# Kernel optimization log

Measured on AMD Instinct MI355X. Metric: run time of the kernel, lower is better.

Reference implementation:

```python
import jax, jax.numpy as jnp
from jax import lax
import numpy as np

GROUPS = 4


def _grid_sample_border(img, gx, gy):
    # img: [Bg, Cg, H, W]; gx, gy: [Bg, H, W] normalized grid in [-1, 1]
    # Replicates F.grid_sample(mode='bilinear', align_corners=False, padding_mode='border')
    Bg, Cg, H, W = img.shape
    ix = jnp.clip(((gx + 1.0) * W - 1.0) * 0.5, 0.0, W - 1.0)
    iy = jnp.clip(((gy + 1.0) * H - 1.0) * 0.5, 0.0, H - 1.0)
    x0 = jnp.floor(ix)
    y0 = jnp.floor(iy)
    wx = ix - x0
    wy = iy - y0
    x0i = x0.astype(jnp.int32)
    y0i = y0.astype(jnp.int32)
    x1i = jnp.minimum(x0i + 1, W - 1)
    y1i = jnp.minimum(y0i + 1, H - 1)

    def one(im, x0i, x1i, y0i, y1i, wx, wy):
        v00 = im[:, y0i, x0i]
        v01 = im[:, y0i, x1i]
        v10 = im[:, y1i, x0i]
        v11 = im[:, y1i, x1i]
        return (v00 * (1 - wx) * (1 - wy) + v01 * wx * (1 - wy)
                + v10 * (1 - wx) * wy + v11 * wx * wy)

    return jax.vmap(one)(img, x0i, x1i, y0i, y1i, wx, wy)


def setup_inputs() -> dict:
    key = jax.random.key(0)
    ks = jax.random.split(key, 8)
    B, N, C = 8, 4096, 768
    x = jax.random.normal(ks[0], (B, N, C), dtype=jnp.float32)
    dw_w = jax.random.normal(ks[1], (C, 1, 3, 3), dtype=jnp.float32) * 0.1  # depthwise kernel
    dw_b = jax.random.normal(ks[2], (C,), dtype=jnp.float32) * 0.1
    off_w = jax.random.normal(ks[3], (2 * GROUPS, C), dtype=jnp.float32) * 0.001  # std=0.001 init
    off_b = jnp.zeros((2 * GROUPS,), dtype=jnp.float32)
    wt_w = jax.random.normal(ks[4], (2 * GROUPS, C), dtype=jnp.float32) * 0.02
    wt_b = jnp.zeros((2 * GROUPS,), dtype=jnp.float32)
    offset_list = jnp.zeros((1,), dtype=jnp.int32)
    return {"x": x, "dw_w": dw_w, "dw_b": dw_b, "off_w": off_w, "off_b": off_b,
            "wt_w": wt_w, "wt_b": wt_b, "offset_list": offset_list,
            "patch_h": 64, "patch_w": 64}


def reference(x, dw_w, dw_b, off_w, off_b, wt_w, wt_b, offset_list, patch_h, patch_w):
    B, N, C = x.shape
    H, W = int(patch_h), int(patch_w)
    xi = jnp.transpose(x, (0, 2, 1)).reshape(B, C, H, W)

    # offset head: depthwise 3x3 conv -> GELU -> 1x1 conv to 2*groups channels
    dw = lax.conv_general_dilated(xi, dw_w, (1, 1), ((1, 1), (1, 1)),
                                  dimension_numbers=("NCHW", "OIHW", "NCHW"),
                                  feature_group_count=C)
    dw = jax.nn.gelu(dw + dw_b[None, :, None, None], approximate=False)
    off = jnp.einsum("bchw,oc->bohw", dw, off_w) + off_b[None, :, None, None]

    # weight head: 1x1 conv -> sigmoid
    wt = jax.nn.sigmoid(jnp.einsum("bchw,oc->bohw", xi, wt_w) + wt_b[None, :, None, None])

    off = (off * wt).reshape(B, 2, GROUPS, H, W)
    # fixed cross-shaped shifts: x-comp [0,0,-1,+1], y-comp [-1,+1,0,0]
    shifts = jnp.array([[0.0, 0.0, -1.0, 1.0], [-1.0, 1.0, 0.0, 0.0]],
                       dtype=x.dtype).reshape(1, 2, GROUPS, 1, 1)
    off = off + shifts

    cx = (jnp.arange(W, dtype=x.dtype) + 0.5)[None, None, None, :]  # pixel-center x coords
    cy = (jnp.arange(H, dtype=x.dtype) + 0.5)[None, None, :, None]  # pixel-center y coords
    gx = 2.0 * (cx + off[:, 0]) / W - 1.0  # [B, GROUPS, H, W]
    gy = 2.0 * (cy + off[:, 1]) / H - 1.0

    img = xi.reshape(B * GROUPS, C // GROUPS, H, W)
    samp = _grid_sample_border(img, gx.reshape(B * GROUPS, H, W),
                               gy.reshape(B * GROUPS, H, W))
    out = samp.reshape(B, C, N)
    return jnp.transpose(out, (0, 2, 1))  # [B, N, C]
```

## Files before the change

kernel.cpp:

```cpp
#include <hip/hip_runtime.h>
#include <math.h>

#define BB 8
#define CC 768
#define HH 64
#define WW 64
#define NN 4096
#define GG 4
#define NCHUNK 6
#define CHUNK 128

typedef __attribute__((ext_vector_type(8))) _Float16 half8;
typedef __attribute__((ext_vector_type(4))) float f32x4;

__device__ __forceinline__ float gelu_fast(float v) {
    const float z = 1.5957691216f * v * fmaf(0.044715f, v * v, 1.0f);
    return __fdividef(v, 1.0f + __expf(-z));
}

__global__ __launch_bounds__(128, 4) void dq_conv_mfma(
    const float* __restrict__ x,
    const float* __restrict__ dw_w,
    const float* __restrict__ dw_b,
    const float* __restrict__ off_w,
    const float* __restrict__ wt_w,
    float* __restrict__ offpart)
{
    __shared__ __attribute__((aligned(16))) _Float16 gl[16][144];
    __shared__ __attribute__((aligned(16))) _Float16 xh[16][144];
    const int t = threadIdx.x;
    const int lane = t & 63, wv = t >> 6;
    const int xcd = blockIdx.x & 7;
    const int local = blockIdx.x >> 3;
    const int chunk = local % NCHUNK;
    const int r = xcd * (BB * HH / 8) + local / NCHUNK;
    const int h = r & (HH - 1);
    const int b = r >> 6;
    const int c = chunk * CHUNK + t;

    const int n = lane & 15, kg = lane >> 4;
    const float* wsrc = (wv == 0) ? off_w : wt_w;
    half8 bfrag[4];
#pragma unroll
    for (int kt = 0; kt < 4; ++kt) {
        const bool valid = (n < 8);
        const float* src = wsrc + (valid ? n : 0) * CC + chunk * CHUNK + kt * 32 + kg * 8;
        half8 bf;
#pragma unroll
        for (int j = 0; j < 8; ++j) {
            bf[j] = (_Float16)(valid ? src[j] : 0.f);
        }
        bfrag[kt] = bf;
    }

    float w9[9];
#pragma unroll
    for (int j = 0; j < 9; ++j) w9[j] = dw_w[c * 9 + j];
    const float bias = dw_b[c];
    const bool tv = (h > 0), bv = (h < HH - 1);
    const float wt0 = tv ? w9[0] : 0.f, wt1 = tv ? w9[1] : 0.f, wt2 = tv ? w9[2] : 0.f;
    const float wb0 = bv ? w9[6] : 0.f, wb1 = bv ? w9[7] : 0.f, wb2 = bv ? w9[8] : 0.f;

    const float* base = x + (size_t)b * NN * CC + c;
    const float* rT = base + (size_t)((tv ? h - 1 : 0) * WW) * CC;
    const float* rM = base + (size_t)(h * WW) * CC;
    const float* rB = base + (size_t)((bv ? h + 1 : h) * WW) * CC;

    float cT[8], cM[8], cB[8], nT[8], nM[8], nB[8];
    float pT = 0.f, pM = 0.f, pB = 0.f;

#pragma unroll
    for (int j = 0; j < 8; ++j) {
        const size_t o = (size_t)j * CC;
        cT[j] = rT[o]; cM[j] = rM[o]; cB[j] = rB[o];
    }

#pragma unroll 1
    for (int wb = 0; wb < 8; ++wb) {
        if (wb < 7) {
#pragma unroll
            for (int j = 0; j < 8; ++j) {
                const size_t o = (size_t)(8 + j) * CC;
                nT[j] = rT[o]; nM[j] = rM[o]; nB[j] = rB[o];
            }
        } else {
#pragma unroll
            for (int j = 0; j < 8; ++j) { nT[j] = 0.f; nM[j] = 0.f; nB[j] = 0.f; }
        }
#pragma unroll
        for (int j = 0; j < 8; ++j) {
            const float lT = j ? cT[j - 1] : pT;
            const float lM = j ? cM[j - 1] : pM;
            const float lB = j ? cB[j - 1] : pB;
            const float rTv = (j == 7) ? nT[0] : cT[j + 1];
            const float rMv = (j == 7) ? nM[0] : cM[j + 1];
            const float rBv = (j == 7) ? nB[0] : cB[j + 1];
            const float conv = lT * wt0 + cT[j] * wt1 + rTv * wt2
                             + lM * w9[3] + cM[j] * w9[4] + rMv * w9[5]
                             + lB * wb0 + cB[j] * wb1 + rBv * wb2;
            const int colq = ((wb & 1) << 3) + j;
            gl[colq][t] = (_Float16)gelu_fast(conv + bias);
            xh[colq][t] = (_Float16)cM[j];
        }
        pT = cT[7]; pM = cM[7]; pB = cB[7];
#pragma unroll
        for (int j = 0; j < 8; ++j) { cT[j] = nT[j]; cM[j] = nM[j]; cB[j] = nB[j]; }
        rT += 8 * CC; rM += 8 * CC; rB += 8 * CC;

        if (wb & 1) {
            const int q = wb >> 1;
            __syncthreads();
            f32x4 acc = {0.f, 0.f, 0.f, 0.f};
            if (wv == 0) {
#pragma unroll
                for (int kt = 0; kt < 4; ++kt) {
                    const half8 a = *(const half8*)&gl[n][kt * 32 + kg * 8];
                    acc = __builtin_amdgcn_mfma_f32_16x16x32_f16(a, bfrag[kt], acc, 0, 0, 0);
                }
            } else {
#pragma unroll
                for (int kt = 0; kt < 4; ++kt) {
                    const half8 a = *(const half8*)&xh[n][kt * 32 + kg * 8];
                    acc = __builtin_amdgcn_mfma_f32_16x16x32_f16(a, bfrag[kt], acc, 0, 0, 0);
                }
            }
            if (n < 8) {
                const int plane = chunk * 16 + (wv ? 8 + n : n);
                const size_t gpos = (size_t)(b * NN) + h * WW + q * 16 + kg * 4;
                float4 st; st.x = acc[0]; st.y = acc[1]; st.z = acc[2]; st.w = acc[3];
                *(float4*)&offpart[(size_t)plane * (BB * NN) + gpos] = st;
            }
            if (wb < 7) __syncthreads();
        }
    }
}

__global__ __launch_bounds__(256) void dq_combine(
    const float* __restrict__ offpart,
    const float* __restrict__ off_b,
    const float* __restrict__ wt_b,
    float* __restrict__ ixiy)
{
    const int t = threadIdx.x;
    const int o = t >> 5;
    const int gpos = blockIdx.x * 32 + (t & 31);
    const int b = gpos >> 12;
    const int hw = gpos & 4095;
    const int h = hw >> 6, w = hw & 63;

    float so = 0.f, sw = 0.f;
#pragma unroll
    for (int ch = 0; ch < NCHUNK; ++ch) {
        so += offpart[((size_t)(ch * 16 + o)) * (BB * NN) + gpos];
        sw += offpart[((size_t)(ch * 16 + 8 + o)) * (BB * NN) + gpos];
    }
    const float sig = 1.f / (1.f + __expf(-(sw + wt_b[o])));
    const float val = (so + off_b[o]) * sig;

    if (o < 4) {
        const float shx = (o == 2) ? -1.f : ((o == 3) ? 1.f : 0.f);
        const float ix = fminf(fmaxf((float)w + val + shx, 0.f), (float)(WW - 1));
        ixiy[(b * GG + o) * NN + hw] = ix;
    } else {
        const int g = o - 4;
        const float shy = (g == 0) ? -1.f : ((g == 1) ? 1.f : 0.f);
        const float iy = fminf(fmaxf((float)h + val + shy, 0.f), (float)(HH - 1));
        ixiy[BB * GG * NN + (b * GG + g) * NN + hw] = iy;
    }
}

__global__ __launch_bounds__(192) void dq_sample_vec(
    const float* __restrict__ x,
    const float* __restrict__ ixiy,
    float* __restrict__ out)
{
    __shared__ float ixy[8];
    const int t = threadIdx.x;
    const int p = (blockIdx.x & 7) * (BB * NN / 8) + (blockIdx.x >> 3);
    const int b = p >> 12;
    const int hw = p & 4095;

    if (t < 8) {
        const int g = t & 3;
        const int plane = (t >> 2) * (BB * GG * NN);
        ixy[t] = ixiy[plane + (b * GG + g) * NN + hw];
    }
    __syncthreads();

    const int g = t / 48;
    const float ix = ixy[g], iy = ixy[4 + g];
    const float x0f = floorf(ix), y0f = floorf(iy);
    const float wx = ix - x0f, wy = iy - y0f;
    const int x0 = (int)x0f, y0 = (int)y0f;
    const int x1 = min(x0 + 1, WW - 1), y1 = min(y0 + 1, HH - 1);
    const int c4 = t * 4;
    const float* xb = x + (size_t)b * NN * CC;
    const float4 v00 = *(const float4*)(xb + (size_t)(y0 * WW + x0) * CC + c4);
    const float4 v01 = *(const float4*)(xb + (size_t)(y0 * WW + x1) * CC + c4);
    const float4 v10 = *(const float4*)(xb + (size_t)(y1 * WW + x0) * CC + c4);
    const float4 v11 = *(const float4*)(xb + (size_t)(y1 * WW + x1) * CC + c4);
    const float w00 = (1.f - wx) * (1.f - wy), w01 = wx * (1.f - wy);
    const float w10 = (1.f - wx) * wy,         w11 = wx * wy;
    float4 r;
    r.x = v00.x * w00 + v01.x * w01 + v10.x * w10 + v11.x * w11;
    r.y = v00.y * w00 + v01.y * w01 + v10.y * w10 + v11.y * w11;
    r.z = v00.z * w00 + v01.z * w01 + v10.z * w10 + v11.z * w11;
    r.w = v00.w * w00 + v01.w * w01 + v10.w * w10 + v11.w * w11;
    *(float4*)(out + (size_t)p * CC + c4) = r;
}

__global__ __launch_bounds__(256) void dqshift_offsets_kernel(
    const float* __restrict__ x, const float* __restrict__ dw_w,
    const float* __restrict__ dw_b, const float* __restrict__ off_w,
    const float* __restrict__ off_b, const float* __restrict__ wt_w,
    const float* __restrict__ wt_b, float* __restrict__ ixiy)
{
    const int wave = threadIdx.x >> 6;
    const int lane = threadIdx.x & 63;
    const int p = blockIdx.x * 4 + wave;
    const int b = p >> 12;
    const int hw = p & 4095;
    const int h = hw >> 6;
    const int w = hw & 63;
    const float* xb = x + (size_t)b * NN * CC;
    float accO[8], accW[8];
#pragma unroll
    for (int o = 0; o < 8; ++o) { accO[o] = 0.f; accW[o] = 0.f; }
    for (int k = 0; k < CC / 64; ++k) {
        const int c = lane + (k << 6);
        float conv = 0.f, xc = 0.f;
#pragma unroll
        for (int dy = -1; dy <= 1; ++dy) {
            const int hh = h + dy;
            const bool vy = (hh >= 0) && (hh < HH);
#pragma unroll
            for (int dx = -1; dx <= 1; ++dx) {
                const int ww = w + dx;
                const bool vv = vy && (ww >= 0) && (ww < WW);
                const float tt = vv ? xb[(size_t)(hh * WW + ww) * CC + c] : 0.f;
                if (dy == 0 && dx == 0) xc = tt;
                conv = fmaf(tt, dw_w[c * 9 + (dy + 1) * 3 + (dx + 1)], conv);
            }
        }
        const float gv = conv + dw_b[c];
        const float gle = 0.5f * gv * (1.0f + erff(gv * 0.70710678118654752f));
#pragma unroll
        for (int o = 0; o < 8; ++o) {
            accO[o] = fmaf(gle, off_w[o * CC + c], accO[o]);
            accW[o] = fmaf(xc, wt_w[o * CC + c], accW[o]);
        }
    }
#pragma unroll
    for (int o = 0; o < 8; ++o) {
#pragma unroll
        for (int s = 32; s > 0; s >>= 1) {
            accO[o] += __shfl_xor(accO[o], s, 64);
            accW[o] += __shfl_xor(accW[o], s, 64);
        }
    }
    if (lane == 0) {
        const float shx[4] = {0.f, 0.f, -1.f, 1.f};
        const float shy[4] = {-1.f, 1.f, 0.f, 0.f};
#pragma unroll
        for (int g = 0; g < 4; ++g) {
            const float sx = 1.f / (1.f + expf(-(accW[g] + wt_b[g])));
            const float sy = 1.f / (1.f + expf(-(accW[4 + g] + wt_b[4 + g])));
            const float ox = (accO[g] + off_b[g]) * sx + shx[g];
            const float oy = (accO[4 + g] + off_b[4 + g]) * sy + shy[g];
            const float ix = fminf(fmaxf((float)w + ox, 0.f), (float)(WW - 1));
            const float iy = fminf(fmaxf((float)h + oy, 0.f), (float)(HH - 1));
            const int idx = (b * GG + g) * NN + hw;
            ixiy[idx] = ix;
            ixiy[BB * GG * NN + idx] = iy;
        }
    }
}

__global__ __launch_bounds__(256) void dqshift_sample_kernel(
    const float* __restrict__ x,
    const float* __restrict__ ixiy,
    float* __restrict__ out)
{
    const int p = blockIdx.x;
    const int b = p >> 12;
    const int hw = p & 4095;
    const float* xb = x + (size_t)b * NN * CC;
    float* ob = out + (size_t)p * CC;

#pragma unroll
    for (int k = 0; k < 3; ++k) {
        const int c = threadIdx.x + (k << 8);
        const int g = c / (CC / GG);
        const int idx = (b * GG + g) * NN + hw;
        const float ix = ixiy[idx];
        const float iy = ixiy[BB * GG * NN + idx];
        const float x0f = floorf(ix);
        const float y0f = floorf(iy);
        const float wx = ix - x0f;
        const float wy = iy - y0f;
        const int x0 = (int)x0f;
        const int y0 = (int)y0f;
        const int x1 = min(x0 + 1, WW - 1);
        const int y1 = min(y0 + 1, HH - 1);
        const float* r0 = xb + (size_t)(y0 * WW) * CC + c;
        const float* r1 = xb + (size_t)(y1 * WW) * CC + c;
        const float v00 = r0[(size_t)x0 * CC];
        const float v01 = r0[(size_t)x1 * CC];
        const float v10 = r1[(size_t)x0 * CC];
        const float v11 = r1[(size_t)x1 * CC];
        ob[c] = v00 * (1.f - wx) * (1.f - wy) + v01 * wx * (1.f - wy)
              + v10 * (1.f - wx) * wy + v11 * wx * wy;
    }
}

extern "C" void kernel_launch(void* const* d_in, const int* in_sizes, int n_in,
                              void* d_out, int out_size, void* d_ws, size_t ws_size,
                              hipStream_t stream) {
    const float* x     = (const float*)d_in[0];
    const float* dw_w  = (const float*)d_in[1];
    const float* dw_b  = (const float*)d_in[2];
    const float* off_w = (const float*)d_in[3];
    const float* off_b = (const float*)d_in[4];
    const float* wt_w  = (const float*)d_in[5];
    const float* wt_b  = (const float*)d_in[6];

    float* ixiy = (float*)d_ws;
    float* offpart = (float*)d_ws + 2 * BB * GG * NN;
    const size_t need = (size_t)(2 * BB * GG * NN + NCHUNK * 16 * BB * NN) * 4;

    if (ws_size >= need) {
        dq_conv_mfma<<<BB * HH * NCHUNK, 128, 0, stream>>>(
            x, dw_w, dw_b, off_w, wt_w, offpart);
        dq_combine<<<BB * NN / 32, 256, 0, stream>>>(
            offpart, off_b, wt_b, ixiy);
        dq_sample_vec<<<BB * NN, 192, 0, stream>>>(
            x, ixiy, (float*)d_out);
    } else {
        dqshift_offsets_kernel<<<BB * NN / 4, 256, 0, stream>>>(
            x, dw_w, dw_b, off_w, off_b, wt_w, wt_b, ixiy);
        dqshift_sample_kernel<<<BB * NN, 256, 0, stream>>>(x, ixiy, (float*)d_out);
    }
}
```

Measured before the change: 82.40 us.

## Process two channels per thread and split conv rows into half-width blocks

The depthwise-conv/MFMA kernel now handles 256 channels per block with each thread loading float2 pairs, and splits each image row into two 32-column halves, which need halo loads at the split edge. The grid grows from 3072 to 3072 blocks (3 chunks × 2 halves), the MFMA K loop doubles to 8 tiles, and the combine kernel reads 3 partial chunks instead of 6. GELU now uses exp2 directly. The intent is to widen global loads, halve the partial-sum traffic, and shorten each block's serial column loop, at the cost of more registers per thread and lower launch-bound occupancy.

```diff
diff --git a/kernel.cpp b/kernel.cpp
--- a/kernel.cpp
+++ b/kernel.cpp
@@ -7,18 +7,20 @@
 #define WW 64
 #define NN 4096
 #define GG 4
-#define NCHUNK 6
-#define CHUNK 128
+#define NCHUNK 3
+#define CHUNK 256
 
 typedef __attribute__((ext_vector_type(8))) _Float16 half8;
+typedef __attribute__((ext_vector_type(2))) _Float16 half2f;
 typedef __attribute__((ext_vector_type(4))) float f32x4;
 
 __device__ __forceinline__ float gelu_fast(float v) {
-    const float z = 1.5957691216f * v * fmaf(0.044715f, v * v, 1.0f);
-    return __fdividef(v, 1.0f + __expf(-z));
-}
-
-__global__ __launch_bounds__(128, 4) void dq_conv_mfma(
+    const float z2 = 2.3022223f * v * fmaf(0.044715f, v * v, 1.0f);
+    const float e = __builtin_amdgcn_exp2f(-z2);
+    return __fdividef(v, 1.0f + e);
+}
+
+__global__ __launch_bounds__(128, 3) void dq_conv_mfma(
     const float* __restrict__ x,
     const float* __restrict__ dw_w,
     const float* __restrict__ dw_b,
@@ -26,107 +28,125 @@
     const float* __restrict__ wt_w,
     float* __restrict__ offpart)
 {
-    __shared__ __attribute__((aligned(16))) _Float16 gl[16][144];
-    __shared__ __attribute__((aligned(16))) _Float16 xh[16][144];
+    __shared__ __attribute__((aligned(16))) _Float16 gl[16][272];
+    __shared__ __attribute__((aligned(16))) _Float16 xh[16][272];
     const int t = threadIdx.x;
     const int lane = t & 63, wv = t >> 6;
     const int xcd = blockIdx.x & 7;
-    const int local = blockIdx.x >> 3;
-    const int chunk = local % NCHUNK;
-    const int r = xcd * (BB * HH / 8) + local / NCHUNK;
+    int local = blockIdx.x >> 3;
+    const int chunk = local % 3; local /= 3;
+    const int half = local & 1;  local >>= 1;
+    const int r = xcd * (BB * HH / 8) + local;
     const int h = r & (HH - 1);
     const int b = r >> 6;
-    const int c = chunk * CHUNK + t;
+    const int wstart = half * 32;
+    const int c0 = chunk * CHUNK + 2 * t;
 
     const int n = lane & 15, kg = lane >> 4;
     const float* wsrc = (wv == 0) ? off_w : wt_w;
-    half8 bfrag[4];
-#pragma unroll
-    for (int kt = 0; kt < 4; ++kt) {
+    half8 bfrag[8];
+#pragma unroll
+    for (int kt = 0; kt < 8; ++kt) {
         const bool valid = (n < 8);
         const float* src = wsrc + (valid ? n : 0) * CC + chunk * CHUNK + kt * 32 + kg * 8;
         half8 bf;
 #pragma unroll
-        for (int j = 0; j < 8; ++j) {
-            bf[j] = (_Float16)(valid ? src[j] : 0.f);
-        }
+        for (int j = 0; j < 8; ++j) bf[j] = (_Float16)(valid ? src[j] : 0.f);
         bfrag[kt] = bf;
     }
 
-    float w9[9];
-#pragma unroll
-    for (int j = 0; j < 9; ++j) w9[j] = dw_w[c * 9 + j];
-    const float bias = dw_b[c];
+    float wA[9], wB[9];
+#pragma unroll
+    for (int j = 0; j < 9; ++j) { wA[j] = dw_w[c0 * 9 + j]; wB[j] = dw_w[(c0 + 1) * 9 + j]; }
+    const float biasA = dw_b[c0], biasB = dw_b[c0 + 1];
     const bool tv = (h > 0), bv = (h < HH - 1);
-    const float wt0 = tv ? w9[0] : 0.f, wt1 = tv ? w9[1] : 0.f, wt2 = tv ? w9[2] : 0.f;
-    const float wb0 = bv ? w9[6] : 0.f, wb1 = bv ? w9[7] : 0.f, wb2 = bv ? w9[8] : 0.f;
-
-    const float* base = x + (size_t)b * NN * CC + c;
+    if (!tv) { wA[0] = wA[1] = wA[2] = 0.f; wB[0] = wB[1] = wB[2] = 0.f; }
+    if (!bv) { wA[6] = wA[7] = wA[8] = 0.f; wB[6] = wB[7] = wB[8] = 0.f; }
+
+    const float* base = x + (size_t)b * NN * CC + c0;
     const float* rT = base + (size_t)((tv ? h - 1 : 0) * WW) * CC;
     const float* rM = base + (size_t)(h * WW) * CC;
     const float* rB = base + (size_t)((bv ? h + 1 : h) * WW) * CC;
 
-    float cT[8], cM[8], cB[8], nT[8], nM[8], nB[8];
-    float pT = 0.f, pM = 0.f, pB = 0.f;
-
-#pragma unroll
-    for (int j = 0; j < 8; ++j) {
-        const size_t o = (size_t)j * CC;
-        cT[j] = rT[o]; cM[j] = rM[o]; cB[j] = rB[o];
-    }
-
-#pragma unroll 1
+    float2 cT[4], cM[4], cB[4], nT[4], nM[4], nB[4];
+    float2 pT, pM, pB;
+    const float2 zz = make_float2(0.f, 0.f);
+    if (half) {
+        const size_t o = (size_t)(wstart - 1) * CC;
+        pT = *(const float2*)&rT[o]; pM = *(const float2*)&rM[o]; pB = *(const float2*)&rB[o];
+    } else { pT = zz; pM = zz; pB = zz; }
+    float2 tT, tM, tB;
+    if (!half) {
+        const size_t o = (size_t)(wstart + 32) * CC;
+        tT = *(const float2*)&rT[o]; tM = *(const float2*)&rM[o]; tB = *(const float2*)&rB[o];
+    } else { tT = zz; tM = zz; tB = zz; }
+
+#pragma unroll
+    for (int j = 0; j < 4; ++j) {
+        const size_t o = (size_t)(wstart + j) * CC;
+        cT[j] = *(const float2*)&rT[o]; cM[j] = *(const float2*)&rM[o]; cB[j] = *(const float2*)&rB[o];
+    }
+
+#pragma unroll
     for (int wb = 0; wb < 8; ++wb) {
         if (wb < 7) {
 #pragma unroll
-            for (int j = 0; j < 8; ++j) {
-                const size_t o = (size_t)(8 + j) * CC;
-                nT[j] = rT[o]; nM[j] = rM[o]; nB[j] = rB[o];
+            for (int j = 0; j < 4; ++j) {
+                const size_t o = (size_t)(wstart + wb * 4 + 4 + j) * CC;
+                nT[j] = *(const float2*)&rT[o];
+                nM[j] = *(const float2*)&rM[o];
+                nB[j] = *(const float2*)&rB[o];
             }
         } else {
-#pragma unroll
-            for (int j = 0; j < 8; ++j) { nT[j] = 0.f; nM[j] = 0.f; nB[j] = 0.f; }
-        }
-#pragma unroll
-        for (int j = 0; j < 8; ++j) {
-            const float lT = j ? cT[j - 1] : pT;
-            const float lM = j ? cM[j - 1] : pM;
-            const float lB = j ? cB[j - 1] : pB;
-            const float rTv = (j == 7) ? nT[0] : cT[j + 1];
-            const float rMv = (j == 7) ? nM[0] : cM[j + 1];
-            const float rBv = (j == 7) ? nB[0] : cB[j + 1];
-            const float conv = lT * wt0 + cT[j] * wt1 + rTv * wt2
-                             + lM * w9[3] + cM[j] * w9[4] + rMv * w9[5]
-                             + lB * wb0 + cB[j] * wb1 + rBv * wb2;
-            const int colq = ((wb & 1) << 3) + j;
-            gl[colq][t] = (_Float16)gelu_fast(conv + bias);
-            xh[colq][t] = (_Float16)cM[j];
-        }
-        pT = cT[7]; pM = cM[7]; pB = cB[7];
-#pragma unroll
-        for (int j = 0; j < 8; ++j) { cT[j] = nT[j]; cM[j] = nM[j]; cB[j] = nB[j]; }
-        rT += 8 * CC; rM += 8 * CC; rB += 8 * CC;
-
-        if (wb & 1) {
-            const int q = wb >> 1;
+            nT[0] = tT; nM[0] = tM; nB[0] = tB;
+#pragma unroll
+            for (int j = 1; j < 4; ++j) { nT[j] = zz; nM[j] = zz; nB[j] = zz; }
+        }
+#pragma unroll
+        for (int j = 0; j < 4; ++j) {
+            const float2 lT = j ? cT[j - 1] : pT;
+            const float2 lM = j ? cM[j - 1] : pM;
+            const float2 lB = j ? cB[j - 1] : pB;
+            const float2 rTv = (j == 3) ? nT[0] : cT[j + 1];
+            const float2 rMv = (j == 3) ? nM[0] : cM[j + 1];
+            const float2 rBv = (j == 3) ? nB[0] : cB[j + 1];
+            const float convA = lT.x * wA[0] + cT[j].x * wA[1] + rTv.x * wA[2]
+                              + lM.x * wA[3] + cM[j].x * wA[4] + rMv.x * wA[5]
+                              + lB.x * wA[6] + cB[j].x * wA[7] + rBv.x * wA[8];
+            const float convB = lT.y * wB[0] + cT[j].y * wB[1] + rTv.y * wB[2]
+                              + lM.y * wB[3] + cM[j].y * wB[4] + rMv.y * wB[5]
+                              + lB.y * wB[6] + cB[j].y * wB[7] + rBv.y * wB[8];
+            const int colq = (wb & 3) * 4 + j;
+            half2f gv; gv[0] = (_Float16)gelu_fast(convA + biasA);
+                       gv[1] = (_Float16)gelu_fast(convB + biasB);
+            *(half2f*)&gl[colq][2 * t] = gv;
+            half2f xv; xv[0] = (_Float16)cM[j].x; xv[1] = (_Float16)cM[j].y;
+            *(half2f*)&xh[colq][2 * t] = xv;
+        }
+        pT = cT[3]; pM = cM[3]; pB = cB[3];
+#pragma unroll
+        for (int j = 0; j < 4; ++j) { cT[j] = nT[j]; cM[j] = nM[j]; cB[j] = nB[j]; }
+
+        if ((wb & 3) == 3) {
+            const int q = wb >> 2;
             __syncthreads();
             f32x4 acc = {0.f, 0.f, 0.f, 0.f};
             if (wv == 0) {
 #pragma unroll
-                for (int kt = 0; kt < 4; ++kt) {
+                for (int kt = 0; kt < 8; ++kt) {
                     const half8 a = *(const half8*)&gl[n][kt * 32 + kg * 8];
                     acc = __builtin_amdgcn_mfma_f32_16x16x32_f16(a, bfrag[kt], acc, 0, 0, 0);
                 }
             } else {
 #pragma unroll
-                for (int kt = 0; kt < 4; ++kt) {
+                for (int kt = 0; kt < 8; ++kt) {
                     const half8 a = *(const half8*)&xh[n][kt * 32 + kg * 8];
                     acc = __builtin_amdgcn_mfma_f32_16x16x32_f16(a, bfrag[kt], acc, 0, 0, 0);
                 }
             }
             if (n < 8) {
                 const int plane = chunk * 16 + (wv ? 8 + n : n);
-                const size_t gpos = (size_t)(b * NN) + h * WW + q * 16 + kg * 4;
+                const size_t gpos = (size_t)(b * NN) + h * WW + wstart + q * 16 + kg * 4;
                 float4 st; st.x = acc[0]; st.y = acc[1]; st.z = acc[2]; st.w = acc[3];
                 *(float4*)&offpart[(size_t)plane * (BB * NN) + gpos] = st;
             }
@@ -201,12 +221,12 @@
     const float4 v11 = *(const float4*)(xb + (size_t)(y1 * WW + x1) * CC + c4);
     const float w00 = (1.f - wx) * (1.f - wy), w01 = wx * (1.f - wy);
     const float w10 = (1.f - wx) * wy,         w11 = wx * wy;
-    float4 r;
-    r.x = v00.x * w00 + v01.x * w01 + v10.x * w10 + v11.x * w11;
-    r.y = v00.y * w00 + v01.y * w01 + v10.y * w10 + v11.y * w11;
-    r.z = v00.z * w00 + v01.z * w01 + v10.z * w10 + v11.z * w11;
-    r.w = v00.w * w00 + v01.w * w01 + v10.w * w10 + v11.w * w11;
-    *(float4*)(out + (size_t)p * CC + c4) = r;
+    float4 rr;
+    rr.x = v00.x * w00 + v01.x * w01 + v10.x * w10 + v11.x * w11;
+    rr.y = v00.y * w00 + v01.y * w01 + v10.y * w10 + v11.y * w11;
+    rr.z = v00.z * w00 + v01.z * w01 + v10.z * w10 + v11.z * w11;
+    rr.w = v00.w * w00 + v01.w * w01 + v10.w * w10 + v11.w * w11;
+    *(float4*)(out + (size_t)p * CC + c4) = rr;
 }
 
 __global__ __launch_bounds__(256) void dqshift_offsets_kernel(
@@ -329,7 +349,7 @@
     const size_t need = (size_t)(2 * BB * GG * NN + NCHUNK * 16 * BB * NN) * 4;
 
     if (ws_size >= need) {
-        dq_conv_mfma<<<BB * HH * NCHUNK, 128, 0, stream>>>(
+        dq_conv_mfma<<<BB * HH * NCHUNK * 2, 128, 0, stream>>>(
             x, dw_w, dw_b, off_w, wt_w, offpart);
         dq_combine<<<BB * NN / 32, 256, 0, stream>>>(
             offpart, off_b, wt_b, ixiy);
```

After: 88.49 us. +7.4%, slower.
